# Performance work log

Hardware: AMD Instinct MI355X
Metric: run time of the kernel (lower is better)

The kernel has to match this reference:

```python
import jax, jax.numpy as jnp
import numpy as np

N_NODES = 100000
N_EDGES = 1600000
F_IN = 128
HID = 128


def setup_inputs() -> dict:
    key = jax.random.key(0)
    ks = jax.random.split(key, 16)
    x = jax.random.normal(ks[0], (N_NODES, F_IN), dtype=jnp.float32)
    edge_index = jax.random.randint(ks[1], (2, N_EDGES), 0, N_NODES, dtype=jnp.int32)
    edge_weight = jax.random.uniform(ks[2], (N_EDGES,), dtype=jnp.float32)
    def glorot(k, fan_in, fan_out):
        s = jnp.sqrt(6.0 / (fan_in + fan_out))
        return jax.random.uniform(k, (fan_in, fan_out), dtype=jnp.float32, minval=-s, maxval=s)
    inp = {"x": x, "edge_index": edge_index, "edge_weight": edge_weight}
    dims = [(F_IN, HID), (HID, HID), (HID, HID), (HID, HID)]
    for i, (di, do) in enumerate(dims):
        inp[f"Wc{i}"] = glorot(ks[3 + i], di, do)
        inp[f"bc{i}"] = jnp.zeros((do,), dtype=jnp.float32)
    inp["Wout"] = glorot(ks[8], HID, F_IN)
    inp["bout"] = jnp.zeros((F_IN,), dtype=jnp.float32)
    return inp


def _gcn_conv(x, W, b, row, col, ew, deg_isqrt, n):
    # PyG GCNConv: h = x @ W; out = sum_{(r,c)} norm_rc * h[r] scattered to c, plus
    # self-loop term (weight 1), plus bias. norm_rc = d^-1/2[r] * ew * d^-1/2[c].
    h = x @ W
    norm = deg_isqrt[row] * ew * deg_isqrt[col]          # [E]
    agg = jax.ops.segment_sum(h[row] * norm[:, None], col, num_segments=n)
    agg = agg + h * (deg_isqrt * deg_isqrt)[:, None]      # self loops, weight 1
    return agg + b


def reference(x, edge_index, edge_weight, Wc0, bc0, Wc1, bc1, Wc2, bc2, Wc3, bc3, Wout, bout):
    n = x.shape[0]
    row, col = edge_index[0], edge_index[1]
    # degree includes self-loop weight 1 (gcn_norm with add_self_loops=True)
    deg = jax.ops.segment_sum(edge_weight, col, num_segments=n) + 1.0
    deg_isqrt = jnp.where(deg > 0, jax.lax.rsqrt(deg), 0.0)
    Ws = [Wc0, Wc1, Wc2, Wc3]
    bs = [bc0, bc1, bc2, bc3]
    h = x
    for i in range(3):
        h = jax.nn.relu(_gcn_conv(h, Ws[i], bs[i], row, col, edge_weight, deg_isqrt, n))
    h = _gcn_conv(h, Ws[3], bs[3], row, col, edge_weight, deg_isqrt, n)
    return h @ Wout + bout
```

## Files before the change

kernel.cpp:

```cpp
#include <hip/hip_runtime.h>


#define SCAN_CHUNK 1024
#define NBUCK_MAX  512
#define BCAP       6144

typedef __attribute__((ext_vector_type(8))) short bf16x8;
typedef __attribute__((ext_vector_type(4))) float f32x4;

__device__ inline unsigned bf16pack(float a, float b) {
    unsigned ua = __float_as_uint(a);
    unsigned ub = __float_as_uint(b);
    ua = (ua + 0x7fffu + ((ua >> 16) & 1u)) >> 16;
    ub = (ub + 0x7fffu + ((ub >> 16) & 1u)) & 0xffff0000u;
    return ua | ub;
}

__device__ inline void split2(float x, ushort& hi, ushort& lo) {
    unsigned u = __float_as_uint(x);
    unsigned r = (u + 0x7fffu + ((u >> 16) & 1u)) & 0xffff0000u;
    hi = (ushort)(r >> 16);
    float rem = x - __uint_as_float(r);
    unsigned u2 = __float_as_uint(rem);
    lo = (ushort)((u2 + 0x7fffu + ((u2 >> 16) & 1u)) >> 16);
}

__device__ inline void bf16x8_expand(uint4 w, float4& a, float4& b) {
    a.x = __uint_as_float(w.x << 16);
    a.y = __uint_as_float(w.x & 0xffff0000u);
    a.z = __uint_as_float(w.y << 16);
    a.w = __uint_as_float(w.y & 0xffff0000u);
    b.x = __uint_as_float(w.z << 16);
    b.y = __uint_as_float(w.z & 0xffff0000u);
    b.z = __uint_as_float(w.w << 16);
    b.w = __uint_as_float(w.w & 0xffff0000u);
}

__global__ __launch_bounds__(256) void k_prepw(const float* W0, const float* W1,
                                               const float* W2, const float* W3,
                                               const float* W4,
                                               ushort* __restrict__ hiO,
                                               ushort* __restrict__ loO) {
    const float* W = (blockIdx.x == 0) ? W0 : (blockIdx.x == 1) ? W1 :
                     (blockIdx.x == 2) ? W2 : (blockIdx.x == 3) ? W3 : W4;
    ushort* h = hiO + (size_t)blockIdx.x * 16384;
    ushort* l = loO + (size_t)blockIdx.x * 16384;
    for (int idx = threadIdx.x; idx < 4096; idx += 256) {
        int n  = idx >> 5;
        int kq = (idx & 31) * 4;
        ushort hs[4], ls[4];
#pragma unroll
        for (int j = 0; j < 4; j++) split2(W[(kq + j) * 128 + n], hs[j], ls[j]);
        *(uint2*)&h[n * 128 + kq] =
            make_uint2(hs[0] | ((unsigned)hs[1] << 16), hs[2] | ((unsigned)hs[3] << 16));
        *(uint2*)&l[n * 128 + kq] =
            make_uint2(ls[0] | ((unsigned)ls[1] << 16), ls[2] | ((unsigned)ls[3] << 16));
    }
}

__global__ __launch_bounds__(256) void k_hist(const int* __restrict__ col,
                                              int* __restrict__ hist,
                                              int E, int K, int B1, int chunk) {
    __shared__ int cnt[NBUCK_MAX];
    int b = blockIdx.x, t = threadIdx.x;
    for (int k = t; k < K; k += 256) cnt[k] = 0;
    __syncthreads();
    int e0 = b * chunk, e1 = min(e0 + chunk, E);
    for (int e = e0 + t; e < e1; e += 256) atomicAdd(&cnt[col[e] >> 8], 1);
    __syncthreads();
    for (int k = t; k < K; k += 256) hist[k * B1 + b] = cnt[k];
}

__global__ __launch_bounds__(256) void k_scan_part(const int* __restrict__ count,
                                                   int* __restrict__ partials, int n) {
    __shared__ int red[256];
    int t = threadIdx.x;
    int base = blockIdx.x * SCAN_CHUNK + t * 4;
    int s = 0;
#pragma unroll
    for (int j = 0; j < 4; j++) {
        int i = base + j;
        if (i < n) s += count[i];
    }
    red[t] = s;
    __syncthreads();
    for (int off = 128; off > 0; off >>= 1) {
        if (t < off) red[t] += red[t + off];
        __syncthreads();
    }
    if (t == 0) partials[blockIdx.x] = red[0];
}

__global__ __launch_bounds__(1024) void k_scan_top(const int* __restrict__ partials,
                                                   int* __restrict__ blockOff,
                                                   int* __restrict__ result,
                                                   int nb, int n) {
    __shared__ int sums[1024];
    int t = threadIdx.x;
    int v = (t < nb) ? partials[t] : 0;
    sums[t] = v;
    __syncthreads();
    for (int off = 1; off < 1024; off <<= 1) {
        int u = (t >= off) ? sums[t - off] : 0;
        __syncthreads();
        sums[t] += u;
        __syncthreads();
    }
    if (t < nb) blockOff[t] = sums[t] - v;
    if (t == nb - 1) result[n] = sums[t];
}

__global__ __launch_bounds__(256) void k_scan_out(const int* __restrict__ count,
                                                  const int* __restrict__ blockOff,
                                                  int* __restrict__ result, int n) {
    __shared__ int sums[256];
    int t = threadIdx.x;
    int base = blockIdx.x * SCAN_CHUNK + t * 4;
    int c[4]; int s = 0;
#pragma unroll
    for (int j = 0; j < 4; j++) {
        int i = base + j;
        c[j] = (i < n) ? count[i] : 0;
        s += c[j];
    }
    sums[t] = s;
    __syncthreads();
    for (int off = 1; off < 256; off <<= 1) {
        int u = (t >= off) ? sums[t - off] : 0;
        __syncthreads();
        sums[t] += u;
        __syncthreads();
    }
    int run = blockOff[blockIdx.x] + sums[t] - s;
#pragma unroll
    for (int j = 0; j < 4; j++) {
        int i = base + j;
        if (i < n) result[i] = run;
        run += c[j];
    }
}

__global__ __launch_bounds__(256) void k_scatter(const int* __restrict__ row,
                                                 const int* __restrict__ col,
                                                 const float* __restrict__ ew,
                                                 const int* __restrict__ binBase,
                                                 uint2* __restrict__ etmp,
                                                 int E, int K, int B1, int chunk) {
    __shared__ int cur[NBUCK_MAX];
    int b = blockIdx.x, t = threadIdx.x;
    for (int k = t; k < K; k += 256) cur[k] = binBase[k * B1 + b];
    __syncthreads();
    int e0 = b * chunk, e1 = min(e0 + chunk, E);
    for (int e = e0 + t; e < e1; e += 256) {
        int c = col[e];
        int k = c >> 8;
        int pos = atomicAdd(&cur[k], 1);
        etmp[pos] = make_uint2((unsigned)row[e] | ((unsigned)(c & 255) << 24),
                               __float_as_uint(ew[e]));
    }
}

__global__ __launch_bounds__(256) void k_bucket(const uint2* __restrict__ etmp,
                                                const int* __restrict__ binBase,
                                                uint2* __restrict__ edges,
                                                int* __restrict__ offsets,
                                                float* __restrict__ disq,
                                                int N, int K, int B1) {
    __shared__ unsigned ls[BCAP];
    __shared__ unsigned lw[BCAP];
    __shared__ int   cnt[256];
    __shared__ float sew[256];
    __shared__ int   excl[257];
    int k = blockIdx.x, t = threadIdx.x;
    int bStart = binBase[k * B1];
    int bEnd   = binBase[(k + 1) * B1];
    int size   = bEnd - bStart;
    cnt[t] = 0; sew[t] = 0.f;
    __syncthreads();
    for (int i = t; i < size && i < BCAP; i += 256) {
        uint2 m = etmp[bStart + i];
        ls[i] = m.x; lw[i] = m.y;
        int j = m.x >> 24;
        atomicAdd(&cnt[j], 1);
        atomicAdd(&sew[j], __uint_as_float(m.y));
    }
    __syncthreads();
    excl[t + 1] = cnt[t];
    if (t == 0) excl[0] = 0;
    __syncthreads();
    for (int off = 1; off < 256; off <<= 1) {
        int add = (t + 1 > off) ? excl[t + 1 - off] : 0;
        __syncthreads();
        excl[t + 1] += add;
        __syncthreads();
    }
    int node = (k << 8) + t;
    if (node < N) {
        offsets[node] = bStart + excl[t];
        disq[node]    = rsqrtf(1.0f + sew[t]);
    }
    if (k == K - 1 && t == 0) offsets[N] = bEnd;
    cnt[t] = excl[t];
    __syncthreads();
    for (int i = t; i < size && i < BCAP; i += 256) {
        unsigned s = ls[i];
        int j = s >> 24;
        int pos = atomicAdd(&cnt[j], 1);
        edges[bStart + pos] = make_uint2(s & 0x00FFFFFFu, lw[i]);
    }
}

template <bool BF16OUT>
__global__ __launch_bounds__(256) void k_gemm_mfma(const float* __restrict__ A,
                                                   const ushort* __restrict__ WThi,
                                                   const ushort* __restrict__ WTlo,
                                                   const float* __restrict__ bias,
                                                   const float* __restrict__ disq,
                                                   void* __restrict__ Cout, int N) {
    __shared__ ushort Whi_s[128][136];
    __shared__ ushort Wlo_s[128][136];
    int tid = threadIdx.x;
#pragma unroll
    for (int r = 0; r < 8; r++) {
        int n  = r * 16 + (tid >> 4);
        int kq = (tid & 15) * 8;
        *(uint4*)&Whi_s[n][kq] = *(const uint4*)&WThi[n * 128 + kq];
        *(uint4*)&Wlo_s[n][kq] = *(const uint4*)&WTlo[n * 128 + kq];
    }
    __syncthreads();

    int wv = tid >> 6, ln = tid & 63;
    int quad = ln >> 4, col = ln & 15;
    int nodeBase = blockIdx.x * 128 + wv * 32;
    int node0 = nodeBase + col, node1 = nodeBase + 16 + col;

    f32x4 acc[2][8];
#pragma unroll
    for (int nb = 0; nb < 2; nb++)
#pragma unroll
        for (int f = 0; f < 8; f++) acc[nb][f] = (f32x4)0.f;

    for (int s = 0; s < 4; s++) {
        int k0 = s * 32 + quad * 8;
        float v0[8], v1[8];
#pragma unroll
        for (int j = 0; j < 8; j++) { v0[j] = 0.f; v1[j] = 0.f; }
        if (node0 < N) {
            float4 a = *(const float4*)&A[(size_t)node0 * 128 + k0];
            float4 b = *(const float4*)&A[(size_t)node0 * 128 + k0 + 4];
            v0[0] = a.x; v0[1] = a.y; v0[2] = a.z; v0[3] = a.w;
            v0[4] = b.x; v0[5] = b.y; v0[6] = b.z; v0[7] = b.w;
        }
        if (node1 < N) {
            float4 a = *(const float4*)&A[(size_t)node1 * 128 + k0];
            float4 b = *(const float4*)&A[(size_t)node1 * 128 + k0 + 4];
            v1[0] = a.x; v1[1] = a.y; v1[2] = a.z; v1[3] = a.w;
            v1[4] = b.x; v1[5] = b.y; v1[6] = b.z; v1[7] = b.w;
        }
        bf16x8 bh0, bl0, bh1, bl1;
#pragma unroll
        for (int j = 0; j < 8; j++) {
            ushort h, l;
            split2(v0[j], h, l); bh0[j] = (short)h; bl0[j] = (short)l;
            split2(v1[j], h, l); bh1[j] = (short)h; bl1[j] = (short)l;
        }
#pragma unroll
        for (int f = 0; f < 8; f++) {
            bf16x8 wh = *(const bf16x8*)&Whi_s[f * 16 + col][k0];
            bf16x8 wl = *(const bf16x8*)&Wlo_s[f * 16 + col][k0];
            acc[0][f] = __builtin_amdgcn_mfma_f32_16x16x32_bf16(wh, bh0, acc[0][f], 0, 0, 0);
            acc[1][f] = __builtin_amdgcn_mfma_f32_16x16x32_bf16(wh, bh1, acc[1][f], 0, 0, 0);
            acc[0][f] = __builtin_amdgcn_mfma_f32_16x16x32_bf16(wl, bh0, acc[0][f], 0, 0, 0);
            acc[1][f] = __builtin_amdgcn_mfma_f32_16x16x32_bf16(wl, bh1, acc[1][f], 0, 0, 0);
            acc[0][f] = __builtin_amdgcn_mfma_f32_16x16x32_bf16(wh, bl0, acc[0][f], 0, 0, 0);
            acc[1][f] = __builtin_amdgcn_mfma_f32_16x16x32_bf16(wh, bl1, acc[1][f], 0, 0, 0);
        }
    }
#pragma unroll
    for (int nb = 0; nb < 2; nb++) {
        int node = nodeBase + nb * 16 + col;
        if (node >= N) continue;
        if (BF16OUT) {
            float d = disq[node];
            unsigned* tb = (unsigned*)Cout;
#pragma unroll
            for (int f = 0; f < 8; f++) {
                f32x4 a = acc[nb][f];
                uint2 u;
                u.x = bf16pack(a[0] * d, a[1] * d);
                u.y = bf16pack(a[2] * d, a[3] * d);
                *(uint2*)&tb[(size_t)node * 64 + f * 8 + quad * 2] = u;
            }
        } else {
            float* C = (float*)Cout;
#pragma unroll
            for (int f = 0; f < 8; f++) {
                int fb = f * 16 + quad * 4;
                float4 bv = *(const float4*)&bias[fb];
                f32x4 a = acc[nb][f];
                float4 o;
                o.x = a[0] + bv.x; o.y = a[1] + bv.y;
                o.z = a[2] + bv.z; o.w = a[3] + bv.w;
                *(float4*)&C[(size_t)node * 128 + fb] = o;
            }
        }
    }
}

__global__ __launch_bounds__(256) void k_aggregate(const unsigned* __restrict__ tb,
                                                   const int* __restrict__ offsets,
                                                   const uint2* __restrict__ edges,
                                                   const float* __restrict__ disq,
                                                   const float* __restrict__ bias,
                                                   float* __restrict__ out,
                                                   int N, int relu) {
    int wave = threadIdx.x >> 6;
    int lane = threadIdx.x & 63;
    int node = blockIdx.x * 4 + wave;
    if (node >= N) return;
    int q  = lane >> 4;
    int li = lane & 15;

    float4 acc0 = make_float4(0.f, 0.f, 0.f, 0.f);
    float4 acc1 = make_float4(0.f, 0.f, 0.f, 0.f);

    int e0 = offsets[node], e1 = offsets[node + 1];
    for (int eb = e0; eb < e1; eb += 64) {
        int n_e = min(64, e1 - eb);
        int src_l = 0; float coef_l = 0.f;
        if (lane < n_e) {
            uint2 m = edges[eb + lane];
            src_l  = (int)m.x;
            coef_l = __uint_as_float(m.y);
        }
        int i = 0;
        for (; i + 16 <= n_e; i += 16) {
            int   s0 = __shfl(src_l,  i + q);
            int   s1 = __shfl(src_l,  i + 4 + q);
            int   s2 = __shfl(src_l,  i + 8 + q);
            int   s3 = __shfl(src_l,  i + 12 + q);
            float n0 = __shfl(coef_l, i + q);
            float n1 = __shfl(coef_l, i + 4 + q);
            float n2 = __shfl(coef_l, i + 8 + q);
            float n3 = __shfl(coef_l, i + 12 + q);
            uint4 w0 = *(const uint4*)&tb[(size_t)s0 * 64 + li * 4];
            uint4 w1 = *(const uint4*)&tb[(size_t)s1 * 64 + li * 4];
            uint4 w2 = *(const uint4*)&tb[(size_t)s2 * 64 + li * 4];
            uint4 w3 = *(const uint4*)&tb[(size_t)s3 * 64 + li * 4];
            float4 a, b;
            bf16x8_expand(w0, a, b);
            acc0.x += n0 * a.x; acc0.y += n0 * a.y; acc0.z += n0 * a.z; acc0.w += n0 * a.w;
            acc1.x += n0 * b.x; acc1.y += n0 * b.y; acc1.z += n0 * b.z; acc1.w += n0 * b.w;
            bf16x8_expand(w1, a, b);
            acc0.x += n1 * a.x; acc0.y += n1 * a.y; acc0.z += n1 * a.z; acc0.w += n1 * a.w;
            acc1.x += n1 * b.x; acc1.y += n1 * b.y; acc1.z += n1 * b.z; acc1.w += n1 * b.w;
            bf16x8_expand(w2, a, b);
            acc0.x += n2 * a.x; acc0.y += n2 * a.y; acc0.z += n2 * a.z; acc0.w += n2 * a.w;
            acc1.x += n2 * b.x; acc1.y += n2 * b.y; acc1.z += n2 * b.z; acc1.w += n2 * b.w;
            bf16x8_expand(w3, a, b);
            acc0.x += n3 * a.x; acc0.y += n3 * a.y; acc0.z += n3 * a.z; acc0.w += n3 * a.w;
            acc1.x += n3 * b.x; acc1.y += n3 * b.y; acc1.z += n3 * b.z; acc1.w += n3 * b.w;
        }
        for (; i < n_e; i += 4) {
            int idx = i + q; if (idx > 63) idx = 63;
            int   s0 = __shfl(src_l,  idx);
            float n0 = __shfl(coef_l, idx);
            uint4 w0 = *(const uint4*)&tb[(size_t)s0 * 64 + li * 4];
            float4 a, b;
            bf16x8_expand(w0, a, b);
            acc0.x += n0 * a.x; acc0.y += n0 * a.y; acc0.z += n0 * a.z; acc0.w += n0 * a.w;
            acc1.x += n0 * b.x; acc1.y += n0 * b.y; acc1.z += n0 * b.z; acc1.w += n0 * b.w;
        }
    }
#pragma unroll
    for (int m = 16; m <= 32; m <<= 1) {
        acc0.x += __shfl_xor(acc0.x, m);
        acc0.y += __shfl_xor(acc0.y, m);
        acc0.z += __shfl_xor(acc0.z, m);
        acc0.w += __shfl_xor(acc0.w, m);
        acc1.x += __shfl_xor(acc1.x, m);
        acc1.y += __shfl_xor(acc1.y, m);
        acc1.z += __shfl_xor(acc1.z, m);
        acc1.w += __shfl_xor(acc1.w, m);
    }
    if (q == 0) {
        float d = disq[node];
        uint4 wv = *(const uint4*)&tb[(size_t)node * 64 + li * 4];
        float4 ta, tbv;
        bf16x8_expand(wv, ta, tbv);
        float4 b0 = *(const float4*)&bias[li * 8];
        float4 b1 = *(const float4*)&bias[li * 8 + 4];
        float4 o0, o1;
        o0.x = d * (acc0.x + ta.x) + b0.x;
        o0.y = d * (acc0.y + ta.y) + b0.y;
        o0.z = d * (acc0.z + ta.z) + b0.z;
        o0.w = d * (acc0.w + ta.w) + b0.w;
        o1.x = d * (acc1.x + tbv.x) + b1.x;
        o1.y = d * (acc1.y + tbv.y) + b1.y;
        o1.z = d * (acc1.z + tbv.z) + b1.z;
        o1.w = d * (acc1.w + tbv.w) + b1.w;
        if (relu) {
            o0.x = fmaxf(o0.x, 0.f); o0.y = fmaxf(o0.y, 0.f);
            o0.z = fmaxf(o0.z, 0.f); o0.w = fmaxf(o0.w, 0.f);
            o1.x = fmaxf(o1.x, 0.f); o1.y = fmaxf(o1.y, 0.f);
            o1.z = fmaxf(o1.z, 0.f); o1.w = fmaxf(o1.w, 0.f);
        }
        *(float4*)&out[(size_t)node * 128 + li * 8]     = o0;
        *(float4*)&out[(size_t)node * 128 + li * 8 + 4] = o1;
    }
}

extern "C" void kernel_launch(void* const* d_in, const int* in_sizes, int n_in,
                              void* d_out, int out_size, void* d_ws, size_t ws_size,
                              hipStream_t stream) {
    const float* x    = (const float*)d_in[0];
    const int*   ei   = (const int*)d_in[1];
    const float* ew   = (const float*)d_in[2];
    const float* Wc[4] = {(const float*)d_in[3], (const float*)d_in[5],
                          (const float*)d_in[7], (const float*)d_in[9]};
    const float* bc[4] = {(const float*)d_in[4], (const float*)d_in[6],
                          (const float*)d_in[8], (const float*)d_in[10]};
    const float* Wout = (const float*)d_in[11];
    const float* bout = (const float*)d_in[12];

    const int N = in_sizes[0] / 128;
    const int E = in_sizes[2];
    const int* row = ei;
    const int* col = ei + E;

    const int K     = (N + 255) >> 8;
    const int B1    = 256;
    const int chunk = (E + B1 - 1) / B1;
    const int nScan = K * B1;

    size_t off = 0;
    char* base = (char*)d_ws;
    auto alloc = [&](size_t bytes) -> void* {
        void* p = base + off;
        off += (bytes + 255) & ~(size_t)255;
        return p;
    };
    float*    disq     = (float*)alloc((size_t)N * 4);
    int*      offsets  = (int*)alloc((size_t)(N + 1) * 4);
    int*      hist     = (int*)alloc((size_t)nScan * 4);
    int*      binBase  = (int*)alloc((size_t)(nScan + 1) * 4);
    int*      partials = (int*)alloc(1024 * 4);
    int*      blockOff = (int*)alloc(1024 * 4);
    ushort*   WThi     = (ushort*)alloc((size_t)5 * 16384 * 2);
    ushort*   WTlo     = (ushort*)alloc((size_t)5 * 16384 * 2);
    uint2*    etmp     = (uint2*)alloc((size_t)E * 8);
    uint2*    edges    = (uint2*)alloc((size_t)E * 8);
    float*    h        = (float*)alloc((size_t)N * 128 * 4);
    unsigned* tb       = (unsigned*)alloc((size_t)N * 64 * 4);

    const int BG  = (N + 127) / 128;
    const int BA  = (N + 3) / 4;
    const int NBs = (nScan + SCAN_CHUNK - 1) / SCAN_CHUNK;

    k_prepw<<<5, 256, 0, stream>>>(Wc[0], Wc[1], Wc[2], Wc[3], Wout, WThi, WTlo);
    k_hist<<<B1, 256, 0, stream>>>(col, hist, E, K, B1, chunk);
    k_scan_part<<<NBs, 256, 0, stream>>>(hist, partials, nScan);
    k_scan_top<<<1, 1024, 0, stream>>>(partials, blockOff, binBase, NBs, nScan);
    k_scan_out<<<NBs, 256, 0, stream>>>(hist, blockOff, binBase, nScan);
    k_scatter<<<B1, 256, 0, stream>>>(row, col, ew, binBase, etmp, E, K, B1, chunk);
    k_bucket<<<K, 256, 0, stream>>>(etmp, binBase, edges, offsets, disq, N, K, B1);

    k_gemm_mfma<true><<<BG, 256, 0, stream>>>(x, WThi, WTlo, nullptr, disq, tb, N);
    k_aggregate<<<BA, 256, 0, stream>>>(tb, offsets, edges, disq, bc[0], h, N, 1);
    k_gemm_mfma<true><<<BG, 256, 0, stream>>>(h, WThi + 16384, WTlo + 16384, nullptr, disq, tb, N);
    k_aggregate<<<BA, 256, 0, stream>>>(tb, offsets, edges, disq, bc[1], h, N, 1);
    k_gemm_mfma<true><<<BG, 256, 0, stream>>>(h, WThi + 32768, WTlo + 32768, nullptr, disq, tb, N);
    k_aggregate<<<BA, 256, 0, stream>>>(tb, offsets, edges, disq, bc[2], h, N, 1);
    k_gemm_mfma<true><<<BG, 256, 0, stream>>>(h, WThi + 49152, WTlo + 49152, nullptr, disq, tb, N);
    k_aggregate<<<BA, 256, 0, stream>>>(tb, offsets, edges, disq, bc[3], h, N, 0);
    k_gemm_mfma<false><<<BG, 256, 0, stream>>>(h, WThi + 65536, WTlo + 65536, bout, nullptr, d_out, N);
}
```

Baseline: 584.8 us.

## Store intermediate activations in bf16 and software-pipeline the aggregation gather

```diff
diff --git a/kernel.cpp b/kernel.cpp
--- a/kernel.cpp
+++ b/kernel.cpp
@@ -210,13 +210,11 @@
     }
 }
 
-template <bool BF16OUT>
-__global__ __launch_bounds__(256) void k_gemm_mfma(const float* __restrict__ A,
+__global__ __launch_bounds__(256) void k_gemm_f32A(const float* __restrict__ A,
                                                    const ushort* __restrict__ WThi,
                                                    const ushort* __restrict__ WTlo,
-                                                   const float* __restrict__ bias,
                                                    const float* __restrict__ disq,
-                                                   void* __restrict__ Cout, int N) {
+                                                   unsigned* __restrict__ Cout, int N) {
     __shared__ ushort Whi_s[128][136];
     __shared__ ushort Wlo_s[128][136];
     int tid = threadIdx.x;
@@ -280,6 +278,68 @@
     for (int nb = 0; nb < 2; nb++) {
         int node = nodeBase + nb * 16 + col;
         if (node >= N) continue;
+        float d = disq[node];
+#pragma unroll
+        for (int f = 0; f < 8; f++) {
+            f32x4 a = acc[nb][f];
+            uint2 u;
+            u.x = bf16pack(a[0] * d, a[1] * d);
+            u.y = bf16pack(a[2] * d, a[3] * d);
+            *(uint2*)&Cout[(size_t)node * 64 + f * 8 + quad * 2] = u;
+        }
+    }
+}
+
+template <bool BF16OUT>
+__global__ __launch_bounds__(256) void k_gemm_b16A(const unsigned* __restrict__ Ab,
+                                                   const ushort* __restrict__ WThi,
+                                                   const ushort* __restrict__ WTlo,
+                                                   const float* __restrict__ bias,
+                                                   const float* __restrict__ disq,
+                                                   void* __restrict__ Cout, int N) {
+    __shared__ ushort Whi_s[128][136];
+    __shared__ ushort Wlo_s[128][136];
+    int tid = threadIdx.x;
+#pragma unroll
+    for (int r = 0; r < 8; r++) {
+        int n  = r * 16 + (tid >> 4);
+        int kq = (tid & 15) * 8;
+        *(uint4*)&Whi_s[n][kq] = *(const uint4*)&WThi[n * 128 + kq];
+        *(uint4*)&Wlo_s[n][kq] = *(const uint4*)&WTlo[n * 128 + kq];
+    }
+    __syncthreads();
+
+    int wv = tid >> 6, ln = tid & 63;
+    int quad = ln >> 4, col = ln & 15;
+    int nodeBase = blockIdx.x * 128 + wv * 32;
+    int node0 = nodeBase + col, node1 = nodeBase + 16 + col;
+
+    f32x4 acc[2][8];
+#pragma unroll
+    for (int nb = 0; nb < 2; nb++)
+#pragma unroll
+        for (int f = 0; f < 8; f++) acc[nb][f] = (f32x4)0.f;
+
+    for (int s = 0; s < 4; s++) {
+        int k0 = s * 32 + quad * 8;
+        int kw = s * 16 + quad * 4;
+        bf16x8 b0 = (bf16x8)(short)0, b1 = (bf16x8)(short)0;
+        if (node0 < N) b0 = *(const bf16x8*)&Ab[(size_t)node0 * 64 + kw];
+        if (node1 < N) b1 = *(const bf16x8*)&Ab[(size_t)node1 * 64 + kw];
+#pragma unroll
+        for (int f = 0; f < 8; f++) {
+            bf16x8 wh = *(const bf16x8*)&Whi_s[f * 16 + col][k0];
+            bf16x8 wl = *(const bf16x8*)&Wlo_s[f * 16 + col][k0];
+            acc[0][f] = __builtin_amdgcn_mfma_f32_16x16x32_bf16(wh, b0, acc[0][f], 0, 0, 0);
+            acc[1][f] = __builtin_amdgcn_mfma_f32_16x16x32_bf16(wh, b1, acc[1][f], 0, 0, 0);
+            acc[0][f] = __builtin_amdgcn_mfma_f32_16x16x32_bf16(wl, b0, acc[0][f], 0, 0, 0);
+            acc[1][f] = __builtin_amdgcn_mfma_f32_16x16x32_bf16(wl, b1, acc[1][f], 0, 0, 0);
+        }
+    }
+#pragma unroll
+    for (int nb = 0; nb < 2; nb++) {
+        int node = nodeBase + nb * 16 + col;
+        if (node >= N) continue;
         if (BF16OUT) {
             float d = disq[node];
             unsigned* tb = (unsigned*)Cout;
@@ -312,7 +372,7 @@
                                                    const uint2* __restrict__ edges,
                                                    const float* __restrict__ disq,
                                                    const float* __restrict__ bias,
-                                                   float* __restrict__ out,
+                                                   unsigned* __restrict__ outb,
                                                    int N, int relu) {
     int wave = threadIdx.x >> 6;
     int lane = threadIdx.x & 63;
@@ -321,57 +381,49 @@
     int q  = lane >> 4;
     int li = lane & 15;
 
+    int e0 = offsets[node], e1 = offsets[node + 1];
+    int deg = e1 - e0;
     float4 acc0 = make_float4(0.f, 0.f, 0.f, 0.f);
     float4 acc1 = make_float4(0.f, 0.f, 0.f, 0.f);
 
-    int e0 = offsets[node], e1 = offsets[node + 1];
-    for (int eb = e0; eb < e1; eb += 64) {
-        int n_e = min(64, e1 - eb);
-        int src_l = 0; float coef_l = 0.f;
-        if (lane < n_e) {
-            uint2 m = edges[eb + lane];
-            src_l  = (int)m.x;
-            coef_l = __uint_as_float(m.y);
-        }
-        int i = 0;
-        for (; i + 16 <= n_e; i += 16) {
-            int   s0 = __shfl(src_l,  i + q);
-            int   s1 = __shfl(src_l,  i + 4 + q);
-            int   s2 = __shfl(src_l,  i + 8 + q);
-            int   s3 = __shfl(src_l,  i + 12 + q);
-            float n0 = __shfl(coef_l, i + q);
-            float n1 = __shfl(coef_l, i + 4 + q);
-            float n2 = __shfl(coef_l, i + 8 + q);
-            float n3 = __shfl(coef_l, i + 12 + q);
-            uint4 w0 = *(const uint4*)&tb[(size_t)s0 * 64 + li * 4];
-            uint4 w1 = *(const uint4*)&tb[(size_t)s1 * 64 + li * 4];
-            uint4 w2 = *(const uint4*)&tb[(size_t)s2 * 64 + li * 4];
-            uint4 w3 = *(const uint4*)&tb[(size_t)s3 * 64 + li * 4];
-            float4 a, b;
-            bf16x8_expand(w0, a, b);
-            acc0.x += n0 * a.x; acc0.y += n0 * a.y; acc0.z += n0 * a.z; acc0.w += n0 * a.w;
-            acc1.x += n0 * b.x; acc1.y += n0 * b.y; acc1.z += n0 * b.z; acc1.w += n0 * b.w;
-            bf16x8_expand(w1, a, b);
-            acc0.x += n1 * a.x; acc0.y += n1 * a.y; acc0.z += n1 * a.z; acc0.w += n1 * a.w;
-            acc1.x += n1 * b.x; acc1.y += n1 * b.y; acc1.z += n1 * b.z; acc1.w += n1 * b.w;
-            bf16x8_expand(w2, a, b);
-            acc0.x += n2 * a.x; acc0.y += n2 * a.y; acc0.z += n2 * a.z; acc0.w += n2 * a.w;
-            acc1.x += n2 * b.x; acc1.y += n2 * b.y; acc1.z += n2 * b.z; acc1.w += n2 * b.w;
-            bf16x8_expand(w3, a, b);
-            acc0.x += n3 * a.x; acc0.y += n3 * a.y; acc0.z += n3 * a.z; acc0.w += n3 * a.w;
-            acc1.x += n3 * b.x; acc1.y += n3 * b.y; acc1.z += n3 * b.z; acc1.w += n3 * b.w;
-        }
-        for (; i < n_e; i += 4) {
-            int idx = i + q; if (idx > 63) idx = 63;
-            int   s0 = __shfl(src_l,  idx);
-            float n0 = __shfl(coef_l, idx);
-            uint4 w0 = *(const uint4*)&tb[(size_t)s0 * 64 + li * 4];
-            float4 a, b;
-            bf16x8_expand(w0, a, b);
-            acc0.x += n0 * a.x; acc0.y += n0 * a.y; acc0.z += n0 * a.z; acc0.w += n0 * a.w;
-            acc1.x += n0 * b.x; acc1.y += n0 * b.y; acc1.z += n0 * b.z; acc1.w += n0 * b.w;
-        }
-    }
+    int eL = e0 + q;
+    float cf[4];
+    uint4 w[4];
+#pragma unroll
+    for (int s = 0; s < 4; s++) { cf[s] = 0.f; w[s] = make_uint4(0u, 0u, 0u, 0u); }
+
+#define FETCH(S, II) {                                                     \
+        int ii = (II);                                                     \
+        bool v = ii < e1;                                                  \
+        if (v) {                                                           \
+            uint2 m = edges[ii];                                           \
+            cf[S] = __uint_as_float(m.y);                                  \
+            w[S]  = *(const uint4*)&tb[(size_t)m.x * 64 + li * 4];         \
+        } else cf[S] = 0.f;                                                \
+    }
+#define CONSUME(S) {                                                       \
+        float4 a, b; bf16x8_expand(w[S], a, b);                            \
+        float c = cf[S];                                                   \
+        acc0.x += c * a.x; acc0.y += c * a.y;                              \
+        acc0.z += c * a.z; acc0.w += c * a.w;                              \
+        acc1.x += c * b.x; acc1.y += c * b.y;                              \
+        acc1.z += c * b.z; acc1.w += c * b.w;                              \
+    }
+
+    FETCH(0, eL)
+    FETCH(1, eL + 4)
+    FETCH(2, eL + 8)
+    FETCH(3, eL + 12)
+    for (int base = 16; base < deg; base += 16) {
+        CONSUME(0) FETCH(0, eL + base)
+        CONSUME(1) FETCH(1, eL + base + 4)
+        CONSUME(2) FETCH(2, eL + base + 8)
+        CONSUME(3) FETCH(3, eL + base + 12)
+    }
+    CONSUME(0) CONSUME(1) CONSUME(2) CONSUME(3)
+#undef FETCH
+#undef CONSUME
+
 #pragma unroll
     for (int m = 16; m <= 32; m <<= 1) {
         acc0.x += __shfl_xor(acc0.x, m);
@@ -405,8 +457,12 @@
             o1.x = fmaxf(o1.x, 0.f); o1.y = fmaxf(o1.y, 0.f);
             o1.z = fmaxf(o1.z, 0.f); o1.w = fmaxf(o1.w, 0.f);
         }
-        *(float4*)&out[(size_t)node * 128 + li * 8]     = o0;
-        *(float4*)&out[(size_t)node * 128 + li * 8 + 4] = o1;
+        uint4 u;
+        u.x = bf16pack(o0.x, o0.y);
+        u.y = bf16pack(o0.z, o0.w);
+        u.z = bf16pack(o1.x, o1.y);
+        u.w = bf16pack(o1.z, o1.w);
+        *(uint4*)&outb[(size_t)node * 64 + li * 4] = u;
     }
 }
 
@@ -450,7 +506,7 @@
     ushort*   WTlo     = (ushort*)alloc((size_t)5 * 16384 * 2);
     uint2*    etmp     = (uint2*)alloc((size_t)E * 8);
     uint2*    edges    = (uint2*)alloc((size_t)E * 8);
-    float*    h        = (float*)alloc((size_t)N * 128 * 4);
+    unsigned* hb       = (unsigned*)alloc((size_t)N * 64 * 4);
     unsigned* tb       = (unsigned*)alloc((size_t)N * 64 * 4);
 
     const int BG  = (N + 127) / 128;
@@ -465,13 +521,13 @@
     k_scatter<<<B1, 256, 0, stream>>>(row, col, ew, binBase, etmp, E, K, B1, chunk);
     k_bucket<<<K, 256, 0, stream>>>(etmp, binBase, edges, offsets, disq, N, K, B1);
 
-    k_gemm_mfma<true><<<BG, 256, 0, stream>>>(x, WThi, WTlo, nullptr, disq, tb, N);
-    k_aggregate<<<BA, 256, 0, stream>>>(tb, offsets, edges, disq, bc[0], h, N, 1);
-    k_gemm_mfma<true><<<BG, 256, 0, stream>>>(h, WThi + 16384, WTlo + 16384, nullptr, disq, tb, N);
-    k_aggregate<<<BA, 256, 0, stream>>>(tb, offsets, edges, disq, bc[1], h, N, 1);
-    k_gemm_mfma<true><<<BG, 256, 0, stream>>>(h, WThi + 32768, WTlo + 32768, nullptr, disq, tb, N);
-    k_aggregate<<<BA, 256, 0, stream>>>(tb, offsets, edges, disq, bc[2], h, N, 1);
-    k_gemm_mfma<true><<<BG, 256, 0, stream>>>(h, WThi + 49152, WTlo + 49152, nullptr, disq, tb, N);
-    k_aggregate<<<BA, 256, 0, stream>>>(tb, offsets, edges, disq, bc[3], h, N, 0);
-    k_gemm_mfma<false><<<BG, 256, 0, stream>>>(h, WThi + 65536, WTlo + 65536, bout, nullptr, d_out, N);
-}
+    k_gemm_f32A<<<BG, 256, 0, stream>>>(x, WThi, WTlo, disq, tb, N);
+    k_aggregate<<<BA, 256, 0, stream>>>(tb, offsets, edges, disq, bc[0], hb, N, 1);
+    k_gemm_b16A<true><<<BG, 256, 0, stream>>>(hb, WThi + 16384, WTlo + 16384, nullptr, disq, tb, N);
+    k_aggregate<<<BA, 256, 0, stream>>>(tb, offsets, edges, disq, bc[1], hb, N, 1);
+    k_gemm_b16A<true><<<BG, 256, 0, stream>>>(hb, WThi + 32768, WTlo + 32768, nullptr, disq, tb, N);
+    k_aggregate<<<BA, 256, 0, stream>>>(tb, offsets, edges, disq, bc[2], hb, N, 1);
+    k_gemm_b16A<true><<<BG, 256, 0, stream>>>(hb, WThi + 49152, WTlo + 49152, nullptr, disq, tb, N);
+    k_aggregate<<<BA, 256, 0, stream>>>(tb, offsets, edges, disq, bc[3], hb, N, 0);
+    k_gemm_b16A<false><<<BG, 256, 0, stream>>>(hb, WThi + 65536, WTlo + 65536, bout, nullptr, d_out, N);
+}
```

New measurement: 581.4 us. Within noise of the previous version (-0.6%).
